# Optimization experiments

Measured on AMD Instinct MI355X. Metric: run time of the kernel, lower is better.

Reference implementation:

```python
import jax, jax.numpy as jnp
import numpy as np

IN_F, OUT_F, RANK, ALPHA = 4096, 4096, 8, 32.0

def setup_inputs() -> dict:
    key = jax.random.key(0)
    kx, kw, ka, kb, kbias = jax.random.split(key, 5)
    x = jax.random.normal(kx, (4, 2048, IN_F), dtype=jnp.float32)
    weight = jax.random.normal(kw, (OUT_F, IN_F), dtype=jnp.float32) * 0.02
    a = jax.random.normal(ka, (OUT_F, RANK), dtype=jnp.float32) * 0.02
    b = jax.random.normal(kb, (RANK, IN_F), dtype=jnp.float32) * 0.02  # zeros in init; use randn for nontrivial test
    bias = jax.random.normal(kbias, (OUT_F,), dtype=jnp.float32) * 0.02
    return {"x": x, "weight": weight, "a": a, "b": b, "bias": bias}

def reference(x, weight, a, b, bias):
    # F.linear(x, W, bias) + F.linear(x, a @ b) * alpha / r
    base = jnp.einsum('bsi,oi->bso', x, weight) + bias
    # low-rank path computed in factored form (same math as x @ (a@b).T)
    lora = jnp.einsum('bsr,or->bso', jnp.einsum('bsi,ri->bsr', x, b), a)
    return base + lora * (ALPHA / RANK)
```

## Files before the change

kernel.cpp:

```cpp
#include <hip/hip_runtime.h>
#include <stdint.h>

#define IN_F 4096
#define OUT_F 4096
#define M_TOT 8192
#define LORA_SCALE 4.0f

typedef unsigned short u16;
typedef __attribute__((ext_vector_type(8))) short bf16x8;
typedef __attribute__((ext_vector_type(4))) float f32x4;

__device__ __forceinline__ u16 f2bf(float f) {
  union { float f; unsigned u; } v; v.f = f;
  unsigned r = v.u + 0x7FFFu + ((v.u >> 16) & 1u);
  return (u16)(r >> 16);
}

__device__ __forceinline__ void gload_lds16(const void* g, void* l) {
  __builtin_amdgcn_global_load_lds(
      (const __attribute__((address_space(1))) void*)g,
      (__attribute__((address_space(3))) void*)l, 16, 0, 0);
}

__global__ void merge_weight(const float* __restrict__ W,
                             const float* __restrict__ A,
                             const float* __restrict__ B,
                             u16* __restrict__ Wb) {
  int idx = blockIdx.x * blockDim.x + threadIdx.x;
  int o  = idx >> 10;
  int i0 = (idx & 1023) << 2;
  const float4 w = *(const float4*)(W + (size_t)o * IN_F + i0);
  float a0 = w.x, a1 = w.y, a2 = w.z, a3 = w.w;
#pragma unroll
  for (int r = 0; r < 8; ++r) {
    float ar = A[o * 8 + r] * LORA_SCALE;
    const float4 bv = *(const float4*)(B + (size_t)r * IN_F + i0);
    a0 += ar * bv.x; a1 += ar * bv.y; a2 += ar * bv.z; a3 += ar * bv.w;
  }
  uint2 pk;
  pk.x = (unsigned)f2bf(a0) | ((unsigned)f2bf(a1) << 16);
  pk.y = (unsigned)f2bf(a2) | ((unsigned)f2bf(a3) << 16);
  *(uint2*)(Wb + (size_t)o * IN_F + i0) = pk;
}

__global__ void convert_x(const float* __restrict__ X, u16* __restrict__ Xb) {
  size_t base = ((size_t)blockIdx.x * blockDim.x + threadIdx.x) * 8;
  float4 v0 = *(const float4*)(X + base);
  float4 v1 = *(const float4*)(X + base + 4);
  uint4 pk;
  pk.x = (unsigned)f2bf(v0.x) | ((unsigned)f2bf(v0.y) << 16);
  pk.y = (unsigned)f2bf(v0.z) | ((unsigned)f2bf(v0.w) << 16);
  pk.z = (unsigned)f2bf(v1.x) | ((unsigned)f2bf(v1.y) << 16);
  pk.w = (unsigned)f2bf(v1.z) | ((unsigned)f2bf(v1.w) << 16);
  *(uint4*)(Xb + base) = pk;
}

__global__ __launch_bounds__(256) void gemm_bias(const u16* __restrict__ Xb,
                                                 const u16* __restrict__ Wb,
                                                 const float* __restrict__ bias,
                                                 float* __restrict__ out) {
  __shared__ __align__(16) u16 ldsA[128 * 64];
  __shared__ __align__(16) u16 ldsB[128 * 64];

  const int tid  = threadIdx.x;
  const int wid  = tid >> 6;
  const int lane = tid & 63;
  const int nt = blockIdx.x & 31;
  const int mt = blockIdx.x >> 5;
  const int m0 = mt * 128, n0 = nt * 128;
  const int wr = wid >> 1, wc = wid & 1;
  const int lr = lane & 15;
  const int kg = lane >> 4;

  const int srow   = wid * 8 + (lane >> 3);
  const int schunk = (lane & 7) ^ (srow & 7);
  const u16* aSrc = Xb + (size_t)(m0 + srow) * IN_F + schunk * 8;
  const u16* bSrc = Wb + (size_t)(n0 + srow) * IN_F + schunk * 8;

  f32x4 acc[4][4] = {};

  for (int kt = 0; kt < IN_F; kt += 64) {
    __syncthreads();
#pragma unroll
    for (int j = 0; j < 4; ++j) {
      gload_lds16(aSrc + (size_t)(j * 32) * IN_F + kt, &ldsA[j * 2048 + wid * 512]);
      gload_lds16(bSrc + (size_t)(j * 32) * IN_F + kt, &ldsB[j * 2048 + wid * 512]);
    }
    __syncthreads();

#pragma unroll
    for (int s = 0; s < 2; ++s) {
      bf16x8 af[4], bfr[4];
#pragma unroll
      for (int m = 0; m < 4; ++m) {
        int r = wr * 64 + m * 16 + lr;
        int c = (s * 4 + kg) ^ (r & 7);
        af[m] = *(const bf16x8*)&ldsA[r * 64 + c * 8];
      }
#pragma unroll
      for (int n = 0; n < 4; ++n) {
        int r = wc * 64 + n * 16 + lr;
        int c = (s * 4 + kg) ^ (r & 7);
        bfr[n] = *(const bf16x8*)&ldsB[r * 64 + c * 8];
      }
#pragma unroll
      for (int m = 0; m < 4; ++m)
#pragma unroll
        for (int n = 0; n < 4; ++n)
          acc[m][n] = __builtin_amdgcn_mfma_f32_16x16x32_bf16(af[m], bfr[n], acc[m][n], 0, 0, 0);
    }
  }

  float bv[4];
#pragma unroll
  for (int n = 0; n < 4; ++n) bv[n] = bias[n0 + wc * 64 + n * 16 + lr];
  const int rbase = m0 + wr * 64 + kg * 4;
#pragma unroll
  for (int m = 0; m < 4; ++m)
#pragma unroll
    for (int n = 0; n < 4; ++n) {
      int col = n0 + wc * 64 + n * 16 + lr;
#pragma unroll
      for (int r = 0; r < 4; ++r)
        out[(size_t)(rbase + m * 16 + r) * OUT_F + col] = acc[m][n][r] + bv[n];
    }
}

__global__ void lora_t(const float* __restrict__ x, const float* __restrict__ B,
                       float* __restrict__ t) {
  int m = blockIdx.x;
  int tid = threadIdx.x, lane = tid & 63;
  float p[8] = {0, 0, 0, 0, 0, 0, 0, 0};
  for (int k = tid; k < IN_F; k += 256) {
    float xv = x[(size_t)m * IN_F + k];
#pragma unroll
    for (int r = 0; r < 8; ++r) p[r] += xv * B[r * IN_F + k];
  }
#pragma unroll
  for (int r = 0; r < 8; ++r) {
    float v = p[r];
    for (int off = 32; off; off >>= 1) v += __shfl_down(v, off);
    if (lane == 0) atomicAdd(&t[m * 8 + r], v);
  }
}

__global__ void fb_gemm(const float* __restrict__ x, const float* __restrict__ W,
                        const float* __restrict__ A, const float* __restrict__ bias,
                        const float* __restrict__ t, float* __restrict__ out) {
  __shared__ float sx[64][17];
  __shared__ float sw[64][17];
  int tx = threadIdx.x, ty = threadIdx.y;
  int tid = ty * 16 + tx;
  int m0 = blockIdx.y * 64, n0 = blockIdx.x * 64;
  float acc[4][4] = {};
  for (int kt = 0; kt < IN_F; kt += 16) {
    __syncthreads();
#pragma unroll
    for (int q = 0; q < 4; ++q) {
      int idx = q * 256 + tid;
      int r = idx >> 4, c = idx & 15;
      sx[r][c] = x[(size_t)(m0 + r) * IN_F + kt + c];
      sw[r][c] = W[(size_t)(n0 + r) * IN_F + kt + c];
    }
    __syncthreads();
#pragma unroll
    for (int k = 0; k < 16; ++k) {
      float xv[4], wv[4];
#pragma unroll
      for (int i = 0; i < 4; ++i) xv[i] = sx[ty * 4 + i][k];
#pragma unroll
      for (int j = 0; j < 4; ++j) wv[j] = sw[tx * 4 + j][k];
#pragma unroll
      for (int i = 0; i < 4; ++i)
#pragma unroll
        for (int j = 0; j < 4; ++j) acc[i][j] += xv[i] * wv[j];
    }
  }
#pragma unroll
  for (int i = 0; i < 4; ++i) {
    int m = m0 + ty * 4 + i;
    float tv[8];
#pragma unroll
    for (int r = 0; r < 8; ++r) tv[r] = t[m * 8 + r];
#pragma unroll
    for (int j = 0; j < 4; ++j) {
      int o = n0 + tx * 4 + j;
      float lora = 0.f;
#pragma unroll
      for (int r = 0; r < 8; ++r) lora += tv[r] * A[o * 8 + r];
      out[(size_t)m * OUT_F + o] = acc[i][j] + bias[o] + LORA_SCALE * lora;
    }
  }
}

extern "C" void kernel_launch(void* const* d_in, const int* in_sizes, int n_in,
                              void* d_out, int out_size, void* d_ws, size_t ws_size,
                              hipStream_t stream) {
  const float* x    = (const float*)d_in[0];
  const float* W    = (const float*)d_in[1];
  const float* A    = (const float*)d_in[2];
  const float* B    = (const float*)d_in[3];
  const float* bias = (const float*)d_in[4];
  float* out = (float*)d_out;

  const size_t xb_elems = (size_t)M_TOT * IN_F;
  const size_t wb_elems = (size_t)OUT_F * IN_F;
  const size_t need = (xb_elems + wb_elems) * sizeof(u16);

  if (ws_size >= need) {
    u16* Xb = (u16*)d_ws;
    u16* Wb = Xb + xb_elems;
    merge_weight<<<(OUT_F * IN_F / 4) / 256, 256, 0, stream>>>(W, A, B, Wb);
    convert_x<<<(M_TOT * IN_F / 8) / 256, 256, 0, stream>>>(x, Xb);
    gemm_bias<<<(M_TOT / 128) * (OUT_F / 128), 256, 0, stream>>>(Xb, Wb, bias, out);
  } else {
    float* t = (float*)d_ws;
    hipMemsetAsync(t, 0, (size_t)M_TOT * 8 * sizeof(float), stream);
    lora_t<<<M_TOT, 256, 0, stream>>>(x, B, t);
    fb_gemm<<<dim3(OUT_F / 64, M_TOT / 64), dim3(16, 16), 0, stream>>>(x, W, A, bias, t, out);
  }
}
```

Before: 352.4 us.

## Add 256x256-tile 8-wave bf16 GEMM with double-buffered LDS pipeline

Adds a new GEMM kernel with 256x256 output tiles, 512 threads and 128KB of dynamic LDS double-buffered across two k-slices. Global-to-LDS loads for the next stage are interleaved with MFMA phases using explicit vmcnt waits, barriers and setprio. Block IDs are swizzled so neighbouring blocks share tiles in cache. It raises data reuse per tile and hides load latency, at the cost of heavy register and LDS use. The old kernel stays as a fallback if the attribute set or launch fails.

Measured after the change: 299.7 us. -14.9%, faster.

```diff
diff --git a/kernel.cpp b/kernel.cpp
--- a/kernel.cpp
+++ b/kernel.cpp
@@ -53,6 +53,125 @@
   pk.z = (unsigned)f2bf(v1.x) | ((unsigned)f2bf(v1.y) << 16);
   pk.w = (unsigned)f2bf(v1.z) | ((unsigned)f2bf(v1.w) << 16);
   *(uint4*)(Xb + base) = pk;
+}
+
+
+#define ABASE(b) ((b) * 32768)
+#define BBASE(b) ((b) * 32768 + 16384)
+
+#define STAGE_A(b, h, kt) do { \
+  gload_lds16(aG + (size_t)((h) * 128) * IN_F + (kt),      lds + ABASE(b) + ((h) * 128) * 64      + tid * 8); \
+  gload_lds16(aG + (size_t)((h) * 128 + 64) * IN_F + (kt), lds + ABASE(b) + ((h) * 128 + 64) * 64 + tid * 8); \
+} while (0)
+
+#define STAGE_B(b, h, kt) do { \
+  gload_lds16(bG + (size_t)((h) * 128) * IN_F + (kt),      lds + BBASE(b) + ((h) * 128) * 64      + tid * 8); \
+  gload_lds16(bG + (size_t)((h) * 128 + 64) * IN_F + (kt), lds + BBASE(b) + ((h) * 128 + 64) * 64 + tid * 8); \
+} while (0)
+
+#define WAIT4 asm volatile("s_waitcnt vmcnt(4)")
+#define WAIT0 asm volatile("s_waitcnt vmcnt(0)")
+
+#define PHASE(b, p, STAGE_STMT, WAIT_STMT) do { \
+  if ((p) == 0) { \
+    _Pragma("unroll") \
+    for (int n = 0; n < 4; ++n) { \
+      Bf0[n] = *(const bf16x8*)(lds + BBASE(b) + (rB + n * 16) * 64 + ck0); \
+      Bf1[n] = *(const bf16x8*)(lds + BBASE(b) + (rB + n * 16) * 64 + ck1); \
+    } \
+  } \
+  bf16x8 a00 = *(const bf16x8*)(lds + ABASE(b) + (rA + (2 * (p)) * 16) * 64 + ck0); \
+  bf16x8 a01 = *(const bf16x8*)(lds + ABASE(b) + (rA + (2 * (p)) * 16) * 64 + ck1); \
+  bf16x8 a10 = *(const bf16x8*)(lds + ABASE(b) + (rA + (2 * (p) + 1) * 16) * 64 + ck0); \
+  bf16x8 a11 = *(const bf16x8*)(lds + ABASE(b) + (rA + (2 * (p) + 1) * 16) * 64 + ck1); \
+  STAGE_STMT; \
+  __builtin_amdgcn_s_barrier(); \
+  asm volatile("s_waitcnt lgkmcnt(0)"); \
+  __builtin_amdgcn_s_setprio(1); \
+  _Pragma("unroll") \
+  for (int n = 0; n < 4; ++n) { \
+    acc[2 * (p)][n]     = __builtin_amdgcn_mfma_f32_16x16x32_bf16(a00, Bf0[n], acc[2 * (p)][n], 0, 0, 0); \
+    acc[2 * (p) + 1][n] = __builtin_amdgcn_mfma_f32_16x16x32_bf16(a10, Bf0[n], acc[2 * (p) + 1][n], 0, 0, 0); \
+  } \
+  _Pragma("unroll") \
+  for (int n = 0; n < 4; ++n) { \
+    acc[2 * (p)][n]     = __builtin_amdgcn_mfma_f32_16x16x32_bf16(a01, Bf1[n], acc[2 * (p)][n], 0, 0, 0); \
+    acc[2 * (p) + 1][n] = __builtin_amdgcn_mfma_f32_16x16x32_bf16(a11, Bf1[n], acc[2 * (p) + 1][n], 0, 0, 0); \
+  } \
+  __builtin_amdgcn_s_setprio(0); \
+  WAIT_STMT; \
+  __builtin_amdgcn_s_barrier(); \
+} while (0)
+
+__global__ __launch_bounds__(512, 2) void gemm8(const u16* __restrict__ Xb,
+                                                const u16* __restrict__ Wb,
+                                                const float* __restrict__ bias,
+                                                float* __restrict__ out) {
+  extern __shared__ u16 lds[];
+
+  const int tid  = threadIdx.x;
+  const int lane = tid & 63;
+  const int wid  = tid >> 6;
+  const int wr = wid >> 2, wc = wid & 3;
+  const int lr = lane & 15, kg = lane >> 4;
+
+  const int bid = blockIdx.x;
+  const int swz = (bid & 7) * 64 + (bid >> 3);
+  const int mt = swz >> 4, nt = swz & 15;
+  const int m0 = mt * 256, n0 = nt * 256;
+
+  const int srow = tid >> 3;
+  const int swc  = (tid & 7) ^ (srow & 7);
+  const u16* aG = Xb + (size_t)(m0 + srow) * IN_F + swc * 8;
+  const u16* bG = Wb + (size_t)(n0 + srow) * IN_F + swc * 8;
+
+  const int rA = wr * 128 + lr;
+  const int rB = wc * 64 + lr;
+  const int ck0 = ((kg) ^ (lane & 7)) * 8;
+  const int ck1 = ((4 + kg) ^ (lane & 7)) * 8;
+
+  f32x4 acc[8][4] = {};
+  bf16x8 Bf0[4], Bf1[4];
+
+  STAGE_B(0, 0, 0); STAGE_B(0, 1, 0);
+  STAGE_A(0, 0, 0); STAGE_A(0, 1, 0);
+  STAGE_B(1, 0, 64); STAGE_B(1, 1, 64);
+  WAIT4;
+  __builtin_amdgcn_s_barrier();
+
+  for (int i = 0; i < 31; ++i) {
+    const int kt1 = i * 128 + 64, kt2 = i * 128 + 128, kt3 = i * 128 + 192;
+    PHASE(0, 0, STAGE_A(1, 0, kt1), );
+    PHASE(0, 1, STAGE_A(1, 1, kt1), );
+    PHASE(0, 2, STAGE_B(0, 0, kt2), );
+    PHASE(0, 3, STAGE_B(0, 1, kt2), WAIT4);
+    PHASE(1, 0, STAGE_A(0, 0, kt2), );
+    PHASE(1, 1, STAGE_A(0, 1, kt2), );
+    PHASE(1, 2, STAGE_B(1, 0, kt3), );
+    PHASE(1, 3, STAGE_B(1, 1, kt3), WAIT4);
+  }
+  PHASE(0, 0, STAGE_A(1, 0, 4032), );
+  PHASE(0, 1, STAGE_A(1, 1, 4032), );
+  PHASE(0, 2, , );
+  PHASE(0, 3, , WAIT0);
+  PHASE(1, 0, , );
+  PHASE(1, 1, , );
+  PHASE(1, 2, , );
+  PHASE(1, 3, , );
+
+  float bv[4];
+#pragma unroll
+  for (int n = 0; n < 4; ++n) bv[n] = bias[n0 + wc * 64 + n * 16 + lr];
+  const int rbase = m0 + wr * 128 + kg * 4;
+#pragma unroll
+  for (int m = 0; m < 8; ++m)
+#pragma unroll
+    for (int n = 0; n < 4; ++n) {
+      int col = n0 + wc * 64 + n * 16 + lr;
+#pragma unroll
+      for (int r = 0; r < 4; ++r)
+        out[(size_t)(rbase + m * 16 + r) * OUT_F + col] = acc[m][n][r] + bv[n];
+    }
 }
 
 __global__ __launch_bounds__(256) void gemm_bias(const u16* __restrict__ Xb,
@@ -212,7 +331,18 @@
     u16* Wb = Xb + xb_elems;
     merge_weight<<<(OUT_F * IN_F / 4) / 256, 256, 0, stream>>>(W, A, B, Wb);
     convert_x<<<(M_TOT * IN_F / 8) / 256, 256, 0, stream>>>(x, Xb);
-    gemm_bias<<<(M_TOT / 128) * (OUT_F / 128), 256, 0, stream>>>(Xb, Wb, bias, out);
+
+    hipError_t e = hipFuncSetAttribute((const void*)gemm8,
+                                       hipFuncAttributeMaxDynamicSharedMemorySize,
+                                       131072);
+    bool used8 = false;
+    if (e == hipSuccess) {
+      gemm8<<<512, 512, 131072, stream>>>(Xb, Wb, bias, out);
+      used8 = (hipGetLastError() == hipSuccess);
+    }
+    if (!used8) {
+      gemm_bias<<<(M_TOT / 128) * (OUT_F / 128), 256, 0, stream>>>(Xb, Wb, bias, out);
+    }
   } else {
     float* t = (float*)d_ws;
     hipMemsetAsync(t, 0, (size_t)M_TOT * 8 * sizeof(float), stream);
```
